# Kernel tuning notes

Measured on AMD Instinct MI355X. Metric: run time of the kernel, lower is better.

Reference implementation:

```python
import jax, jax.numpy as jnp
import numpy as np

N = 50000      # nodes
E = 800000     # edges (avg degree 16)
DF = 128       # node feature dim
EF = 16        # edge feature dim
EH = 64        # edge_filters
NH = 128       # node_filters
C = 40         # classes


def setup_inputs() -> dict:
    key = jax.random.key(0)
    ks = jax.random.split(key, 11)
    s = lambda fan_in: 1.0 / np.sqrt(fan_in)
    return {
        "x": jax.random.normal(ks[0], (N, DF), jnp.float32),
        "edge_feat": jax.random.normal(ks[1], (E, EF), jnp.float32),
        "W1": jax.random.normal(ks[2], (EF, EH), jnp.float32) * s(EF),
        "b1": jnp.zeros((EH,), jnp.float32),
        "W2": jax.random.normal(ks[3], (EH, 1), jnp.float32) * s(EH),
        "b2": jnp.zeros((1,), jnp.float32),
        "Wc1": jax.random.normal(ks[4], (DF, NH), jnp.float32) * s(DF),
        "bc1": jnp.zeros((NH,), jnp.float32),
        "Wc2": jax.random.normal(ks[5], (NH, C), jnp.float32) * s(NH),
        "bc2": jnp.zeros((C,), jnp.float32),
        "edge_index": jax.random.randint(ks[6], (2, E), 0, N, jnp.int32),
    }


def reference(x, edge_feat, W1, b1, W2, b2, Wc1, bc1, Wc2, bc2, edge_index):
    # Edge MLP: per-edge scalar weight in (0, 1)
    eh = jnp.maximum(edge_feat @ W1 + b1, 0.0)          # [E, EH] relu
    ew = jax.nn.sigmoid(eh @ W2 + b2)[:, 0]             # [E]

    # SparseTensor(edges.T, ew, (n, n)): indices are (row=dst, col=src)
    dst = edge_index[0]
    src = edge_index[1]

    # GCNConv 1: relu(A @ (x @ Wc1) + bc1)
    h = x @ Wc1                                         # [N, NH]
    msg = h[src] * ew[:, None]                          # [E, NH] gather
    agg = jax.ops.segment_sum(msg, dst, num_segments=N) # [N, NH] scatter
    h1 = jnp.maximum(agg + bc1, 0.0)
    # dropout(training=False) is identity

    # GCNConv 2: A @ (h1 @ Wc2) + bc2 (linear activation)
    h2 = h1 @ Wc2                                       # [N, C]
    msg2 = h2[src] * ew[:, None]                        # [E, C]
    agg2 = jax.ops.segment_sum(msg2, dst, num_segments=N) + bc2

    return -jax.nn.log_softmax(agg2, axis=1)            # [N, C]
```

## Files before the change

### kernel.cpp

```cpp
#include <hip/hip_runtime.h>
#include <math.h>

#define N_NODES 50000
#define N_EDGES 800000
#define DF 128
#define EF 16
#define EH 64
#define NH 128
#define NC 40
#define NCP 64
#define SCAN_B 196

typedef __attribute__((ext_vector_type(8))) short short8v;
typedef __attribute__((ext_vector_type(4))) short short4v;
typedef __attribute__((ext_vector_type(4))) float f32x4;

__device__ __forceinline__ float bf2f(unsigned short u) {
    union { unsigned int i; float f; } c; c.i = ((unsigned int)u) << 16; return c.f;
}
__device__ __forceinline__ unsigned short f2bf(float f) {
    union { float f; unsigned int i; } c; c.f = f;
    unsigned int r = c.i + 0x7FFFu + ((c.i >> 16) & 1u);
    return (unsigned short)(r >> 16);
}

__global__ __launch_bounds__(256) void edge_mlp_kernel(
    const float* __restrict__ ef, const float* __restrict__ W1,
    const float* __restrict__ b1, const float* __restrict__ W2,
    const float* __restrict__ b2, const int* __restrict__ dst,
    float* __restrict__ ew, int* __restrict__ deg)
{
    int t = threadIdx.x;
    int lane = t & 63;
    int wv = t >> 6;
    int l15 = lane & 15, kg = lane >> 4;

    short8v Bf[4];
    float b1v[4], w2v[4];
    #pragma unroll
    for (int tt = 0; tt < 4; ++tt) {
        int col = tt * 16 + l15;
        short8v bv = {0, 0, 0, 0, 0, 0, 0, 0};
        if (kg < 2) {
            #pragma unroll
            for (int i = 0; i < 8; ++i)
                bv[i] = (short)f2bf(W1[(kg * 8 + i) * EH + col]);
        }
        Bf[tt] = bv;
        b1v[tt] = b1[col];
        w2v[tt] = W2[col];
    }
    float b2s = b2[0];

    long e0w = ((long)blockIdx.x * 4 + wv) * 64;

    #pragma unroll
    for (int rt = 0; rt < 4; ++rt) {
        long e0 = e0w + rt * 16;
        short8v Af = {0, 0, 0, 0, 0, 0, 0, 0};
        if (kg < 2) {
            const float4* p = (const float4*)(ef + (e0 + l15) * EF + kg * 8);
            float4 v0 = p[0], v1 = p[1];
            Af[0] = (short)f2bf(v0.x); Af[1] = (short)f2bf(v0.y);
            Af[2] = (short)f2bf(v0.z); Af[3] = (short)f2bf(v0.w);
            Af[4] = (short)f2bf(v1.x); Af[5] = (short)f2bf(v1.y);
            Af[6] = (short)f2bf(v1.z); Af[7] = (short)f2bf(v1.w);
        }
        f32x4 a0 = {0.f, 0.f, 0.f, 0.f}, a1 = a0, a2 = a0, a3 = a0;
        a0 = __builtin_amdgcn_mfma_f32_16x16x32_bf16(Af, Bf[0], a0, 0, 0, 0);
        a1 = __builtin_amdgcn_mfma_f32_16x16x32_bf16(Af, Bf[1], a1, 0, 0, 0);
        a2 = __builtin_amdgcn_mfma_f32_16x16x32_bf16(Af, Bf[2], a2, 0, 0, 0);
        a3 = __builtin_amdgcn_mfma_f32_16x16x32_bf16(Af, Bf[3], a3, 0, 0, 0);

        float s[4];
        #pragma unroll
        for (int r = 0; r < 4; ++r) {
            s[r] = fmaxf(a0[r] + b1v[0], 0.f) * w2v[0]
                 + fmaxf(a1[r] + b1v[1], 0.f) * w2v[1]
                 + fmaxf(a2[r] + b1v[2], 0.f) * w2v[2]
                 + fmaxf(a3[r] + b1v[3], 0.f) * w2v[3];
            s[r] += __shfl_xor(s[r], 1, 64);
            s[r] += __shfl_xor(s[r], 2, 64);
            s[r] += __shfl_xor(s[r], 4, 64);
            s[r] += __shfl_xor(s[r], 8, 64);
        }
        if (l15 == 0) {
            float4 sg;
            sg.x = 1.f / (1.f + expf(-(s[0] + b2s)));
            sg.y = 1.f / (1.f + expf(-(s[1] + b2s)));
            sg.z = 1.f / (1.f + expf(-(s[2] + b2s)));
            sg.w = 1.f / (1.f + expf(-(s[3] + b2s)));
            *(float4*)(ew + e0 + kg * 4) = sg;
        }
    }
    atomicAdd(&deg[dst[e0w + lane]], 1);
}

__global__ __launch_bounds__(256) void gemm1_kernel(
    const float* __restrict__ x, const float* __restrict__ Wc1,
    unsigned short* __restrict__ hb)
{
    __shared__ float xs[64][DF];
    int t = threadIdx.x;
    long r0 = (long)blockIdx.x * 64;
    for (int i = t; i < 64 * (DF / 4); i += 256) {
        int r = i >> 5, kq = i & 31;
        long rr = r0 + r;
        float4 v = (rr < N_NODES) ? *(const float4*)(x + rr * DF + kq * 4)
                                  : make_float4(0.f, 0.f, 0.f, 0.f);
        *(float4*)(&xs[r][kq * 4]) = v;
    }
    __syncthreads();

    int tr = t >> 5;
    int tc = t & 31;
    float acc[8][4];
    #pragma unroll
    for (int i = 0; i < 8; ++i)
        #pragma unroll
        for (int j = 0; j < 4; ++j) acc[i][j] = 0.f;

    for (int k = 0; k < DF; k += 4) {
        float4 w0 = *(const float4*)(Wc1 + (k + 0) * NH + tc * 4);
        float4 w1 = *(const float4*)(Wc1 + (k + 1) * NH + tc * 4);
        float4 w2 = *(const float4*)(Wc1 + (k + 2) * NH + tc * 4);
        float4 w3 = *(const float4*)(Wc1 + (k + 3) * NH + tc * 4);
        #pragma unroll
        for (int i = 0; i < 8; ++i) {
            float4 xv = *(const float4*)(&xs[tr * 8 + i][k]);
            acc[i][0] += xv.x * w0.x + xv.y * w1.x + xv.z * w2.x + xv.w * w3.x;
            acc[i][1] += xv.x * w0.y + xv.y * w1.y + xv.z * w2.y + xv.w * w3.y;
            acc[i][2] += xv.x * w0.z + xv.y * w1.z + xv.z * w2.z + xv.w * w3.z;
            acc[i][3] += xv.x * w0.w + xv.y * w1.w + xv.z * w2.w + xv.w * w3.w;
        }
    }
    #pragma unroll
    for (int i = 0; i < 8; ++i) {
        long r = r0 + tr * 8 + i;
        if (r < N_NODES) {
            ushort4 sv;
            sv.x = f2bf(acc[i][0]); sv.y = f2bf(acc[i][1]);
            sv.z = f2bf(acc[i][2]); sv.w = f2bf(acc[i][3]);
            *(ushort4*)(hb + r * NH + tc * 4) = sv;
        }
    }
}

__global__ __launch_bounds__(256) void scan_part_kernel(
    const int* __restrict__ deg, int* __restrict__ bsum)
{
    __shared__ int red[256];
    int t = threadIdx.x;
    int n = blockIdx.x * 256 + t;
    red[t] = (n < N_NODES) ? deg[n] : 0;
    __syncthreads();
    for (int o = 128; o > 0; o >>= 1) {
        if (t < o) red[t] += red[t + o];
        __syncthreads();
    }
    if (t == 0) bsum[blockIdx.x] = red[0];
}

__global__ __launch_bounds__(256) void scan_top_kernel(
    const int* __restrict__ bsum, int* __restrict__ boff)
{
    __shared__ int s[256];
    int t = threadIdx.x;
    s[t] = (t < SCAN_B) ? bsum[t] : 0;
    __syncthreads();
    for (int o = 1; o < 256; o <<= 1) {
        int v = (t >= o) ? s[t - o] : 0;
        __syncthreads();
        s[t] += v;
        __syncthreads();
    }
    if (t < SCAN_B) boff[t] = (t == 0) ? 0 : s[t - 1];
}

__global__ __launch_bounds__(256) void scan_write_kernel(
    const int* __restrict__ deg, const int* __restrict__ boff,
    int* __restrict__ rowptr)
{
    __shared__ int s[256];
    int t = threadIdx.x;
    int n = blockIdx.x * 256 + t;
    int v = (n < N_NODES) ? deg[n] : 0;
    s[t] = v;
    __syncthreads();
    for (int o = 1; o < 256; o <<= 1) {
        int u = (t >= o) ? s[t - o] : 0;
        __syncthreads();
        s[t] += u;
        __syncthreads();
    }
    if (n < N_NODES) rowptr[n] = boff[blockIdx.x] + s[t] - v;
}

__global__ __launch_bounds__(256) void fill_csr_kernel(
    const int* __restrict__ dst, const int* __restrict__ src,
    const float* __restrict__ ew, int* __restrict__ rowptr,
    int2* __restrict__ csr)
{
    int e = blockIdx.x * 256 + threadIdx.x;
    if (e >= N_EDGES) return;
    int p = atomicAdd(&rowptr[dst[e]], 1);
    csr[p] = make_int2(src[e], __float_as_int(ew[e]));
}

__global__ __launch_bounds__(256) void gather1_gemm2_kernel(
    const unsigned short* __restrict__ hb, const int* __restrict__ rp_end,
    const int2* __restrict__ csr, const float* __restrict__ bc1,
    const float* __restrict__ Wc2, unsigned short* __restrict__ h2b)
{
    int t = threadIdx.x;
    int node = blockIdx.x * 4 + (t >> 6);
    int lane = t & 63;
    int l16 = lane & 15, g = lane >> 4;

    int end   = rp_end[node];
    int start = (node == 0) ? 0 : rp_end[node - 1];

    float acc[8];
    #pragma unroll
    for (int i = 0; i < 8; ++i) acc[i] = 0.f;

    for (int base = start; base < end; base += 64) {
        int n = end - base; if (n > 64) n = 64;
        int s = 0; float w = 0.f;
        if (lane < n) {
            int2 p = csr[base + lane];
            s = p.x; w = __int_as_float(p.y);
        }
        #pragma unroll 4
        for (int j = 0; j * 4 < n; ++j) {
            int idx = j * 4 + g;
            int   sj = __shfl(s, idx, 64);
            float wj = __shfl(w, idx, 64);
            short8v hv = *(const short8v*)(hb + (long)sj * NH + l16 * 8);
            #pragma unroll
            for (int i = 0; i < 8; ++i)
                acc[i] += wj * bf2f((unsigned short)hv[i]);
        }
    }
    #pragma unroll
    for (int i = 0; i < 8; ++i) {
        acc[i] += __shfl_xor(acc[i], 16, 64);
        acc[i] += __shfl_xor(acc[i], 32, 64);
    }
    float4 b0 = *(const float4*)(bc1 + l16 * 8);
    float4 b1 = *(const float4*)(bc1 + l16 * 8 + 4);
    float h1v[8];
    h1v[0] = fmaxf(acc[0] + b0.x, 0.f); h1v[1] = fmaxf(acc[1] + b0.y, 0.f);
    h1v[2] = fmaxf(acc[2] + b0.z, 0.f); h1v[3] = fmaxf(acc[3] + b0.w, 0.f);
    h1v[4] = fmaxf(acc[4] + b1.x, 0.f); h1v[5] = fmaxf(acc[5] + b1.y, 0.f);
    h1v[6] = fmaxf(acc[6] + b1.z, 0.f); h1v[7] = fmaxf(acc[7] + b1.w, 0.f);

    int c = (lane < NC) ? lane : (NC - 1);
    float o = 0.f;
    #pragma unroll 8
    for (int k = 0; k < NH; ++k) {
        float hk = __shfl(h1v[k & 7], k >> 3, 64);
        o += hk * Wc2[k * NC + c];
    }
    h2b[(long)node * NCP + lane] = f2bf((lane < NC) ? o : 0.f);
}

__global__ __launch_bounds__(256) void gather2_lsm_kernel(
    const unsigned short* __restrict__ h2b, const int* __restrict__ rp_end,
    const int2* __restrict__ csr, const float* __restrict__ bc2,
    float* __restrict__ out)
{
    int t = threadIdx.x;
    int node = blockIdx.x * 4 + (t >> 6);
    int lane = t & 63;
    int l16 = lane & 15, g = lane >> 4;

    int end   = rp_end[node];
    int start = (node == 0) ? 0 : rp_end[node - 1];

    float acc[4];
    #pragma unroll
    for (int i = 0; i < 4; ++i) acc[i] = 0.f;

    for (int base = start; base < end; base += 64) {
        int n = end - base; if (n > 64) n = 64;
        int s = 0; float w = 0.f;
        if (lane < n) {
            int2 p = csr[base + lane];
            s = p.x; w = __int_as_float(p.y);
        }
        #pragma unroll 4
        for (int j = 0; j * 4 < n; ++j) {
            int idx = j * 4 + g;
            int   sj = __shfl(s, idx, 64);
            float wj = __shfl(w, idx, 64);
            short4v hv = *(const short4v*)(h2b + (long)sj * NCP + l16 * 4);
            #pragma unroll
            for (int i = 0; i < 4; ++i)
                acc[i] += wj * bf2f((unsigned short)hv[i]);
        }
    }
    #pragma unroll
    for (int i = 0; i < 4; ++i) {
        acc[i] += __shfl_xor(acc[i], 16, 64);
        acc[i] += __shfl_xor(acc[i], 32, 64);
    }

    bool valid = (l16 < 10);
    float4 bcv = valid ? *(const float4*)(bc2 + l16 * 4) : make_float4(0.f, 0.f, 0.f, 0.f);
    float v[4];
    v[0] = acc[0] + bcv.x; v[1] = acc[1] + bcv.y;
    v[2] = acc[2] + bcv.z; v[3] = acc[3] + bcv.w;

    float mx = valid ? fmaxf(fmaxf(v[0], v[1]), fmaxf(v[2], v[3])) : -INFINITY;
    #pragma unroll
    for (int o = 1; o <= 8; o <<= 1) mx = fmaxf(mx, __shfl_xor(mx, o, 64));
    float se = 0.f;
    if (valid) se = expf(v[0]-mx) + expf(v[1]-mx) + expf(v[2]-mx) + expf(v[3]-mx);
    #pragma unroll
    for (int o = 1; o <= 8; o <<= 1) se += __shfl_xor(se, o, 64);
    float lse = mx + logf(se);

    if (valid && g == 0) {
        float4 r = make_float4(lse - v[0], lse - v[1], lse - v[2], lse - v[3]);
        *(float4*)(out + (long)node * NC + l16 * 4) = r;
    }
}

extern "C" void kernel_launch(void* const* d_in, const int* in_sizes, int n_in,
                              void* d_out, int out_size, void* d_ws, size_t ws_size,
                              hipStream_t stream)
{
    const float* x         = (const float*)d_in[0];
    const float* edge_feat = (const float*)d_in[1];
    const float* W1        = (const float*)d_in[2];
    const float* b1        = (const float*)d_in[3];
    const float* W2        = (const float*)d_in[4];
    const float* b2        = (const float*)d_in[5];
    const float* Wc1       = (const float*)d_in[6];
    const float* bc1       = (const float*)d_in[7];
    const float* Wc2       = (const float*)d_in[8];
    const float* bc2       = (const float*)d_in[9];
    const int*   eidx      = (const int*)d_in[10];
    const int*   dst = eidx;
    const int*   src = eidx + N_EDGES;
    float* out = (float*)d_out;

    float*          ew     = (float*)d_ws;
    unsigned short* hb     = (unsigned short*)(ew + N_EDGES);
    unsigned short* h2b    = hb + (long)N_NODES * NH;
    int2*           csr    = (int2*)(h2b + (long)N_NODES * NCP);
    int*            deg    = (int*)(csr + N_EDGES);
    int*            rowptr = deg + N_NODES;
    int*            bsum   = rowptr + N_NODES;
    int*            boff   = bsum + 256;

    hipMemsetAsync(deg, 0, sizeof(int) * (size_t)N_NODES, stream);

    edge_mlp_kernel<<<N_EDGES / 256, 256, 0, stream>>>(
        edge_feat, W1, b1, W2, b2, dst, ew, deg);
    gemm1_kernel<<<(N_NODES + 63) / 64, 256, 0, stream>>>(x, Wc1, hb);
    scan_part_kernel<<<SCAN_B, 256, 0, stream>>>(deg, bsum);
    scan_top_kernel<<<1, 256, 0, stream>>>(bsum, boff);
    scan_write_kernel<<<SCAN_B, 256, 0, stream>>>(deg, boff, rowptr);
    fill_csr_kernel<<<(N_EDGES + 255) / 256, 256, 0, stream>>>(
        dst, src, ew, rowptr, csr);
    gather1_gemm2_kernel<<<N_NODES / 4, 256, 0, stream>>>(
        hb, rowptr, csr, bc1, Wc2, h2b);
    gather2_lsm_kernel<<<N_NODES / 4, 256, 0, stream>>>(
        h2b, rowptr, csr, bc2, out);
}
```

Before: 350.5 us.

## Use bf16 MFMA for first GEMM and shrink h2 row stride to 40

Rewrites the x@Wc1 GEMM to use 16x16x32 bf16 MFMA instructions, with a small pre-kernel that transposes and converts Wc1 to bf16. The aim is to replace the scalar FP32 FMA loop with matrix cores. The padded 64-wide h2 buffer also becomes 40-wide, and only valid lanes load in the second gather, which cuts gather bandwidth. The cost is that x is now rounded to bf16 before the matmul, which lowers precision.

```diff
diff --git a/kernel.cpp b/kernel.cpp
--- a/kernel.cpp
+++ b/kernel.cpp
@@ -8,7 +8,6 @@
 #define EH 64
 #define NH 128
 #define NC 40
-#define NCP 64
 #define SCAN_B 196
 
 typedef __attribute__((ext_vector_type(8))) short short8v;
@@ -96,52 +95,53 @@
     atomicAdd(&deg[dst[e0w + lane]], 1);
 }
 
+__global__ __launch_bounds__(256) void wc1t_kernel(
+    const float* __restrict__ Wc1, unsigned short* __restrict__ Wc1T)
+{
+    int i = blockIdx.x * 256 + threadIdx.x;
+    int c = i >> 7, k = i & 127;
+    Wc1T[i] = f2bf(Wc1[k * NH + c]);
+}
+
 __global__ __launch_bounds__(256) void gemm1_kernel(
-    const float* __restrict__ x, const float* __restrict__ Wc1,
+    const float* __restrict__ x, const unsigned short* __restrict__ Wc1T,
     unsigned short* __restrict__ hb)
 {
-    __shared__ float xs[64][DF];
-    int t = threadIdx.x;
-    long r0 = (long)blockIdx.x * 64;
-    for (int i = t; i < 64 * (DF / 4); i += 256) {
-        int r = i >> 5, kq = i & 31;
-        long rr = r0 + r;
-        float4 v = (rr < N_NODES) ? *(const float4*)(x + rr * DF + kq * 4)
-                                  : make_float4(0.f, 0.f, 0.f, 0.f);
-        *(float4*)(&xs[r][kq * 4]) = v;
-    }
-    __syncthreads();
-
-    int tr = t >> 5;
-    int tc = t & 31;
-    float acc[8][4];
-    #pragma unroll
-    for (int i = 0; i < 8; ++i)
+    int t = threadIdx.x;
+    int lane = t & 63, wv = t >> 6;
+    int l15 = lane & 15, kg = lane >> 4;
+    long r0w = ((long)blockIdx.x * 4 + wv) * 16;
+    long arow = r0w + l15;
+    bool aok = (arow < N_NODES);
+
+    short8v Af[4];
+    #pragma unroll
+    for (int ks = 0; ks < 4; ++ks) {
+        short8v af = {0, 0, 0, 0, 0, 0, 0, 0};
+        if (aok) {
+            const float4* p = (const float4*)(x + arow * DF + ks * 32 + kg * 8);
+            float4 v0 = p[0], v1 = p[1];
+            af[0] = (short)f2bf(v0.x); af[1] = (short)f2bf(v0.y);
+            af[2] = (short)f2bf(v0.z); af[3] = (short)f2bf(v0.w);
+            af[4] = (short)f2bf(v1.x); af[5] = (short)f2bf(v1.y);
+            af[6] = (short)f2bf(v1.z); af[7] = (short)f2bf(v1.w);
+        }
+        Af[ks] = af;
+    }
+
+    #pragma unroll
+    for (int ct = 0; ct < 8; ++ct) {
+        f32x4 acc = {0.f, 0.f, 0.f, 0.f};
         #pragma unroll
-        for (int j = 0; j < 4; ++j) acc[i][j] = 0.f;
-
-    for (int k = 0; k < DF; k += 4) {
-        float4 w0 = *(const float4*)(Wc1 + (k + 0) * NH + tc * 4);
-        float4 w1 = *(const float4*)(Wc1 + (k + 1) * NH + tc * 4);
-        float4 w2 = *(const float4*)(Wc1 + (k + 2) * NH + tc * 4);
-        float4 w3 = *(const float4*)(Wc1 + (k + 3) * NH + tc * 4);
+        for (int ks = 0; ks < 4; ++ks) {
+            short8v bf = *(const short8v*)(Wc1T + (ct * 16 + l15) * DF + ks * 32 + kg * 8);
+            acc = __builtin_amdgcn_mfma_f32_16x16x32_bf16(Af[ks], bf, acc, 0, 0, 0);
+        }
         #pragma unroll
-        for (int i = 0; i < 8; ++i) {
-            float4 xv = *(const float4*)(&xs[tr * 8 + i][k]);
-            acc[i][0] += xv.x * w0.x + xv.y * w1.x + xv.z * w2.x + xv.w * w3.x;
-            acc[i][1] += xv.x * w0.y + xv.y * w1.y + xv.z * w2.y + xv.w * w3.y;
-            acc[i][2] += xv.x * w0.z + xv.y * w1.z + xv.z * w2.z + xv.w * w3.z;
-            acc[i][3] += xv.x * w0.w + xv.y * w1.w + xv.z * w2.w + xv.w * w3.w;
-        }
-    }
-    #pragma unroll
-    for (int i = 0; i < 8; ++i) {
-        long r = r0 + tr * 8 + i;
-        if (r < N_NODES) {
-            ushort4 sv;
-            sv.x = f2bf(acc[i][0]); sv.y = f2bf(acc[i][1]);
-            sv.z = f2bf(acc[i][2]); sv.w = f2bf(acc[i][3]);
-            *(ushort4*)(hb + r * NH + tc * 4) = sv;
+        for (int r = 0; r < 4; ++r) {
+            long row = r0w + kg * 4 + r;
+            if (row < N_NODES)
+                hb[row * NH + ct * 16 + l15] = f2bf(acc[r]);
         }
     }
 }
@@ -262,7 +262,8 @@
         float hk = __shfl(h1v[k & 7], k >> 3, 64);
         o += hk * Wc2[k * NC + c];
     }
-    h2b[(long)node * NCP + lane] = f2bf((lane < NC) ? o : 0.f);
+    if (lane < NC)
+        h2b[(long)node * NC + lane] = f2bf(o);
 }
 
 __global__ __launch_bounds__(256) void gather2_lsm_kernel(
@@ -274,6 +275,7 @@
     int node = blockIdx.x * 4 + (t >> 6);
     int lane = t & 63;
     int l16 = lane & 15, g = lane >> 4;
+    bool valid = (l16 < 10);
 
     int end   = rp_end[node];
     int start = (node == 0) ? 0 : rp_end[node - 1];
@@ -294,10 +296,12 @@
             int idx = j * 4 + g;
             int   sj = __shfl(s, idx, 64);
             float wj = __shfl(w, idx, 64);
-            short4v hv = *(const short4v*)(h2b + (long)sj * NCP + l16 * 4);
-            #pragma unroll
-            for (int i = 0; i < 4; ++i)
-                acc[i] += wj * bf2f((unsigned short)hv[i]);
+            if (valid) {
+                short4v hv = *(const short4v*)(h2b + (long)sj * NC + l16 * 4);
+                #pragma unroll
+                for (int i = 0; i < 4; ++i)
+                    acc[i] += wj * bf2f((unsigned short)hv[i]);
+            }
         }
     }
     #pragma unroll
@@ -306,7 +310,6 @@
         acc[i] += __shfl_xor(acc[i], 32, 64);
     }
 
-    bool valid = (l16 < 10);
     float4 bcv = valid ? *(const float4*)(bc2 + l16 * 4) : make_float4(0.f, 0.f, 0.f, 0.f);
     float v[4];
     v[0] = acc[0] + bcv.x; v[1] = acc[1] + bcv.y;
@@ -349,17 +352,19 @@
     float*          ew     = (float*)d_ws;
     unsigned short* hb     = (unsigned short*)(ew + N_EDGES);
     unsigned short* h2b    = hb + (long)N_NODES * NH;
-    int2*           csr    = (int2*)(h2b + (long)N_NODES * NCP);
+    int2*           csr    = (int2*)(h2b + (long)N_NODES * NC);
     int*            deg    = (int*)(csr + N_EDGES);
     int*            rowptr = deg + N_NODES;
     int*            bsum   = rowptr + N_NODES;
     int*            boff   = bsum + 256;
+    unsigned short* Wc1T   = (unsigned short*)(boff + 256);
 
     hipMemsetAsync(deg, 0, sizeof(int) * (size_t)N_NODES, stream);
 
+    wc1t_kernel<<<64, 256, 0, stream>>>(Wc1, Wc1T);
     edge_mlp_kernel<<<N_EDGES / 256, 256, 0, stream>>>(
         edge_feat, W1, b1, W2, b2, dst, ew, deg);
-    gemm1_kernel<<<(N_NODES + 63) / 64, 256, 0, stream>>>(x, Wc1, hb);
+    gemm1_kernel<<<(N_NODES + 63) / 64, 256, 0, stream>>>(x, Wc1T, hb);
     scan_part_kernel<<<SCAN_B, 256, 0, stream>>>(deg, bsum);
     scan_top_kernel<<<1, 256, 0, stream>>>(bsum, boff);
     scan_write_kernel<<<SCAN_B, 256, 0, stream>>>(deg, boff, rowptr);
```

After: 346.3 us. No clear change (-1.2%).
